# Kernel tuning notes

Measured on AMD Instinct MI355X. Metric: run time of the kernel, lower is better.

Reference implementation:

```python
import jax, jax.numpy as jnp
import numpy as np

D_MODEL = 1024
HEADS = 16
D_HEAD = D_MODEL // HEADS
LN_EPS = 1e-6


def setup_inputs() -> dict:
    key = jax.random.key(0)
    ks = jax.random.split(key, 7)
    B, S = 4, 2048
    scale = 1.0 / np.sqrt(D_MODEL)
    return {
        "q": jax.random.normal(ks[0], (B, S, D_MODEL), jnp.float32),
        "k": jax.random.normal(ks[1], (B, S, D_MODEL), jnp.float32),
        "v": jax.random.normal(ks[2], (B, S, D_MODEL), jnp.float32),
        "Wq": jax.random.normal(ks[3], (D_MODEL, D_MODEL), jnp.float32) * scale,
        "Wk": jax.random.normal(ks[4], (D_MODEL, D_MODEL), jnp.float32) * scale,
        "Wv": jax.random.normal(ks[5], (D_MODEL, D_MODEL), jnp.float32) * scale,
        "Wo": jax.random.normal(ks[6], (D_MODEL, D_MODEL), jnp.float32) * scale,
        "ln_gamma": jnp.ones((D_MODEL,), jnp.float32),
        "ln_beta": jnp.zeros((D_MODEL,), jnp.float32),
    }


def reference(q, k, v, Wq, Wk, Wv, Wo, ln_gamma, ln_beta):
    B, S, _ = q.shape
    residual = q
    # torch Linear (no bias): y = x @ W.T
    qh = (q @ Wq.T).reshape(B, S, HEADS, D_HEAD).transpose(0, 2, 1, 3)
    kh = (k @ Wk.T).reshape(B, S, HEADS, D_HEAD).transpose(0, 2, 1, 3)
    vh = (v @ Wv.T).reshape(B, S, HEADS, D_HEAD).transpose(0, 2, 1, 3)
    # scaled dot-product attention (no mask, dropout=0)
    att = jnp.einsum("bhsd,bhtd->bhst", qh, kh) / jnp.sqrt(jnp.float32(D_HEAD))
    att = jax.nn.softmax(att, axis=-1)
    ctx = jnp.einsum("bhst,bhtd->bhsd", att, vh)  # (B,H,S,Dh)
    ctx = ctx.transpose(0, 2, 1, 3).reshape(B, S, D_MODEL)
    out = ctx @ Wo.T
    out = out + residual
    # LayerNorm, eps=1e-6
    mu = out.mean(axis=-1, keepdims=True)
    var = out.var(axis=-1, keepdims=True)
    out = (out - mu) * jax.lax.rsqrt(var + LN_EPS) * ln_gamma + ln_beta
    return out
```

## Files before the change

kernel.cpp:

```cpp
#include <hip/hip_runtime.h>
#include <hip/hip_bf16.h>

#define DEVI __device__ __forceinline__

typedef unsigned int u32;
typedef unsigned short u16;
typedef __bf16 bf16_t;
typedef bf16_t bf16x8 __attribute__((ext_vector_type(8)));
typedef bf16_t bf16x4 __attribute__((ext_vector_type(4)));
typedef float f32x4 __attribute__((ext_vector_type(4)));
typedef u32 u32x4 __attribute__((ext_vector_type(4)));
typedef u32 u32x2 __attribute__((ext_vector_type(2)));

DEVI u16 f2bf(float f) {
    u32 u = __builtin_bit_cast(u32, f);
    u = (u + 0x7FFFu + ((u >> 16) & 1u)) >> 16;
    return (u16)u;
}

DEVI u32 pack2bf(float lo, float hi) {
    u32 d;
    asm("v_cvt_pk_bf16_f32 %0, %1, %2" : "=v"(d) : "v"(lo), "v"(hi));
    return d;
}

DEVI float fast_exp2(float x) { return __builtin_amdgcn_exp2f(x); }

typedef __attribute__((address_space(3))) u32 as3_u32;
typedef __attribute__((address_space(1))) u32 as1_u32;

DEVI void gld_lds16(const u16* gsrc, u16* ldst) {
    __builtin_amdgcn_global_load_lds((as1_u32*)gsrc, (as3_u32*)ldst, 16, 0, 0);
}

struct CastArgs {
    const float* src[7];
    u16* dst[7];
    int n[7];
};

__global__ __launch_bounds__(256) void cast_kernel(CastArgs a) {
    int z = blockIdx.y;
    int i = (blockIdx.x * 256 + threadIdx.x) * 8;
    if (i >= a.n[z]) return;
    const float* s = a.src[z] + i;
    float4 f0 = ((const float4*)s)[0];
    float4 f1 = ((const float4*)s)[1];
    u32x4 o;
    o.x = pack2bf(f0.x, f0.y);
    o.y = pack2bf(f0.z, f0.w);
    o.z = pack2bf(f1.x, f1.y);
    o.w = pack2bf(f1.z, f1.w);
    *(u32x4*)(a.dst[z] + i) = o;
}

DEVI void gemm_core(const u16* __restrict__ Ag, const u16* __restrict__ Wg,
                    u16* As, u16* Bs, f32x4 acc[4][4],
                    int tid, int mw, int nw, int q, int cl)
{
    const int K = 1024;
    for (int k0 = 0; k0 < K; k0 += 64) {
        if (k0) __syncthreads();
        #pragma unroll
        for (int pass = 0; pass < 4; ++pass) {
            int id = pass * 256 + tid;
            int r = id >> 3, cp = id & 7, cg = cp ^ (r & 7);
            gld_lds16(Ag + (size_t)r * K + k0 + cg * 8, &As[id * 8]);
            gld_lds16(Wg + (size_t)r * K + k0 + cg * 8, &Bs[id * 8]);
        }
        __syncthreads();
        #pragma unroll
        for (int kh = 0; kh < 2; ++kh) {
            bf16x8 af[4], bfr[4];
            #pragma unroll
            for (int i = 0; i < 4; ++i) {
                int R = mw + i * 16 + cl;
                af[i] = *(const bf16x8*)&As[R * 64 + (((kh * 4 + q) ^ (cl & 7)) * 8)];
            }
            #pragma unroll
            for (int j = 0; j < 4; ++j) {
                int R = nw + j * 16 + cl;
                bfr[j] = *(const bf16x8*)&Bs[R * 64 + (((kh * 4 + q) ^ (cl & 7)) * 8)];
            }
            #pragma unroll
            for (int i = 0; i < 4; ++i)
                #pragma unroll
                for (int j = 0; j < 4; ++j)
                    acc[i][j] = __builtin_amdgcn_mfma_f32_16x16x32_bf16(af[i], bfr[j], acc[i][j], 0, 0, 0);
        }
    }
}

struct QKVArgs { const u16* A[3]; const u16* W[3]; u16* out[3]; };

__global__ __launch_bounds__(256) void qkv_gemm(QKVArgs ga) {
    __shared__ __align__(16) u16 As[128 * 64];
    __shared__ __align__(16) u16 Bs[128 * 64];
    int lin = blockIdx.x;
    int xcd = lin & 7, idx = lin >> 3;
    int wid = xcd * 192 + idx;
    int z = wid >> 9;
    int rem = wid & 511;
    int m0 = (rem >> 3) * 128;
    int n0 = (rem & 7) * 128;

    int tid = threadIdx.x;
    int lane = tid & 63, w = tid >> 6;
    int q = lane >> 4, cl = lane & 15;
    int mw = (w >> 1) * 64, nw = (w & 1) * 64;

    f32x4 acc[4][4] = {};
    const u16* Ag = ga.A[z] + (size_t)m0 * 1024;
    const u16* Wg = ga.W[z] + (size_t)n0 * 1024;
    gemm_core(Ag, Wg, As, Bs, acc, tid, mw, nw, q, cl);

    u16* outb = ga.out[z];
    if (z == 0) {
        const float SC = 0.125f * 1.44269504088896340736f;
        #pragma unroll
        for (int i = 0; i < 4; ++i) {
            int row = m0 + mw + i * 16 + q * 4;
            #pragma unroll
            for (int j = 0; j < 4; ++j) {
                int col = n0 + nw + j * 16 + cl;
                #pragma unroll
                for (int r = 0; r < 4; ++r)
                    outb[(size_t)(row + r) * 1024 + col] = f2bf(acc[i][j][r] * SC);
            }
        }
    } else if (z == 1) {
        #pragma unroll
        for (int i = 0; i < 4; ++i) {
            int row = m0 + mw + i * 16 + q * 4;
            #pragma unroll
            for (int j = 0; j < 4; ++j) {
                int col = n0 + nw + j * 16 + cl;
                #pragma unroll
                for (int r = 0; r < 4; ++r)
                    outb[(size_t)(row + r) * 1024 + col] = f2bf(acc[i][j][r]);
            }
        }
    } else {
        #pragma unroll
        for (int i = 0; i < 4; ++i) {
            int mrow = m0 + mw + i * 16 + q * 4;
            int bb = mrow >> 11, s = mrow & 2047;
            #pragma unroll
            for (int j = 0; j < 4; ++j) {
                int n = n0 + nw + j * 16 + cl;
                u32x2 pk;
                pk.x = pack2bf(acc[i][j][0], acc[i][j][1]);
                pk.y = pack2bf(acc[i][j][2], acc[i][j][3]);
                *(u32x2*)&outb[(size_t)(bb * 1024 + n) * 2048 + s] = pk;
            }
        }
    }
}

__global__ __launch_bounds__(256) void gemm_wo(
    const u16* __restrict__ A, const u16* __restrict__ W,
    float* __restrict__ outf, const float* __restrict__ resid)
{
    __shared__ __align__(16) u16 As[128 * 64];
    __shared__ __align__(16) u16 Bs[128 * 64];
    int lin = blockIdx.x;
    int xcd = lin & 7, idx = lin >> 3;
    int wid = xcd * 64 + idx;
    int m0 = (wid >> 3) * 128;
    int n0 = (wid & 7) * 128;

    int tid = threadIdx.x;
    int lane = tid & 63, w = tid >> 6;
    int q = lane >> 4, cl = lane & 15;
    int mw = (w >> 1) * 64, nw = (w & 1) * 64;

    f32x4 acc[4][4] = {};
    const u16* Ag = A + (size_t)m0 * 1024;
    const u16* Wg = W + (size_t)n0 * 1024;
    gemm_core(Ag, Wg, As, Bs, acc, tid, mw, nw, q, cl);

    #pragma unroll
    for (int i = 0; i < 4; ++i) {
        int row = m0 + mw + i * 16 + q * 4;
        #pragma unroll
        for (int j = 0; j < 4; ++j) {
            int col = n0 + nw + j * 16 + cl;
            #pragma unroll
            for (int r = 0; r < 4; ++r) {
                size_t idx2 = (size_t)(row + r) * 1024 + col;
                outf[idx2] = acc[i][j][r] + resid[idx2];
            }
        }
    }
}


DEVI int kperm64(int r) {
    return (r & 32) | ((r & 12) << 1) | ((r & 16) >> 2) | (r & 3);
}

__global__ __launch_bounds__(256, 4) void attn_kernel(
    const u16* __restrict__ Qp, const u16* __restrict__ Kp,
    const u16* __restrict__ Vt, u16* __restrict__ ctx)
{
    __shared__ __align__(16) u16 Ks[2][64 * 64];
    __shared__ __align__(16) u16 Vs[2][64 * 64];

    int tid = threadIdx.x;
    int lane = tid & 63, w = tid >> 6;
    int q = lane >> 4, cl = lane & 15;

    int linear = blockIdx.x + (blockIdx.y << 4);
    int xcd = linear & 7, j = linear >> 3;
    int bh = xcd * 8 + (j >> 4);
    int qt = j & 15;
    int b = bh >> 4, h = bh & 15;

    const u16* Qg = Qp + (size_t)(b * 2048 + qt * 128) * 1024 + h * 64;
    const u16* Kg = Kp + (size_t)(b * 2048) * 1024 + h * 64;
    const u16* Vg = Vt + (size_t)(b * 1024 + h * 64) * 2048;

    bf16x8 aq[2][2];
    #pragma unroll
    for (int tr = 0; tr < 2; ++tr)
        #pragma unroll
        for (int kk = 0; kk < 2; ++kk)
            aq[tr][kk] = *(const bf16x8*)&Qg[(size_t)(w * 32 + tr * 16 + cl) * 1024 + kk * 32 + q * 8];

    u32x4 ou; ou.x = 0x3F803F80u; ou.y = 0x3F803F80u; ou.z = 0x3F803F80u; ou.w = 0x3F803F80u;
    const bf16x8 ones = __builtin_bit_cast(bf16x8, ou);

    f32x4 oacc[2][4] = {};
    f32x4 lacc[2] = {};

    auto stage = [&](int kt, int bufsel) {
        #pragma unroll
        for (int p = 0; p < 2; ++p) {
            int cid = p * 256 + tid;
            int r = cid >> 3, cp = cid & 7, cg = cp ^ (r & 7);
            gld_lds16(Kg + (size_t)(kt * 64 + kperm64(r)) * 1024 + cg * 8, &Ks[bufsel][cid * 8]);
        }
        #pragma unroll
        for (int p = 0; p < 2; ++p) {
            int cid = p * 256 + tid;
            int r = cid >> 3, cp = cid & 7, cg = cp ^ (r & 7);
            gld_lds16(Vg + (size_t)r * 2048 + kt * 64 + cg * 8, &Vs[bufsel][cid * 8]);
        }
    };

    stage(0, 0);
    asm volatile("s_waitcnt vmcnt(0)" ::: "memory");
    __builtin_amdgcn_s_barrier();
    __builtin_amdgcn_sched_barrier(0);

    for (int kt = 0; kt < 32; ++kt) {
        int cur = kt & 1;
        if (kt < 31) stage(kt + 1, cur ^ 1);
        __builtin_amdgcn_sched_barrier(0);

        const u16* KsC = &Ks[cur][0];
        const u16* VsC = &Vs[cur][0];

        bf16x8 pb[2][2];
        #pragma unroll
        for (int t = 0; t < 2; ++t) {
            int krA = t * 32 + cl, krB = t * 32 + 16 + cl;
            bf16x8 ka0 = *(const bf16x8*)&KsC[krA * 64 + ((q ^ (cl & 7)) * 8)];
            bf16x8 ka1 = *(const bf16x8*)&KsC[krA * 64 + (((4 + q) ^ (cl & 7)) * 8)];
            bf16x8 kb0 = *(const bf16x8*)&KsC[krB * 64 + ((q ^ (cl & 7)) * 8)];
            bf16x8 kb1 = *(const bf16x8*)&KsC[krB * 64 + (((4 + q) ^ (cl & 7)) * 8)];
            #pragma unroll
            for (int tr = 0; tr < 2; ++tr) {
                f32x4 sA = {0.f, 0.f, 0.f, 0.f};
                f32x4 sB = {0.f, 0.f, 0.f, 0.f};
                __builtin_amdgcn_s_setprio(1);
                sA = __builtin_amdgcn_mfma_f32_16x16x32_bf16(ka0, aq[tr][0], sA, 0, 0, 0);
                sA = __builtin_amdgcn_mfma_f32_16x16x32_bf16(ka1, aq[tr][1], sA, 0, 0, 0);
                sB = __builtin_amdgcn_mfma_f32_16x16x32_bf16(kb0, aq[tr][0], sB, 0, 0, 0);
                sB = __builtin_amdgcn_mfma_f32_16x16x32_bf16(kb1, aq[tr][1], sB, 0, 0, 0);
                __builtin_amdgcn_s_setprio(0);
                u32x4 pk;
                pk.x = pack2bf(fast_exp2(sA[0]), fast_exp2(sA[1]));
                pk.y = pack2bf(fast_exp2(sA[2]), fast_exp2(sA[3]));
                pk.z = pack2bf(fast_exp2(sB[0]), fast_exp2(sB[1]));
                pk.w = pack2bf(fast_exp2(sB[2]), fast_exp2(sB[3]));
                pb[tr][t] = __builtin_bit_cast(bf16x8, pk);
            }
        }

        #pragma unroll
        for (int t = 0; t < 2; ++t) {
            #pragma unroll
            for (int td = 0; td < 4; ++td) {
                int d = td * 16 + cl;
                bf16x8 bv = *(const bf16x8*)&VsC[d * 64 + (((t * 4 + q) ^ (cl & 7)) * 8)];
                __builtin_amdgcn_s_setprio(1);
                oacc[0][td] = __builtin_amdgcn_mfma_f32_16x16x32_bf16(pb[0][t], bv, oacc[0][td], 0, 0, 0);
                oacc[1][td] = __builtin_amdgcn_mfma_f32_16x16x32_bf16(pb[1][t], bv, oacc[1][td], 0, 0, 0);
                __builtin_amdgcn_s_setprio(0);
            }
            __builtin_amdgcn_s_setprio(1);
            lacc[0] = __builtin_amdgcn_mfma_f32_16x16x32_bf16(pb[0][t], ones, lacc[0], 0, 0, 0);
            lacc[1] = __builtin_amdgcn_mfma_f32_16x16x32_bf16(pb[1][t], ones, lacc[1], 0, 0, 0);
            __builtin_amdgcn_s_setprio(0);
        }

        asm volatile("s_waitcnt vmcnt(0)" ::: "memory");
        __builtin_amdgcn_s_barrier();
        __builtin_amdgcn_sched_barrier(0);
    }

    u16* Cg = ctx + (size_t)(b * 2048 + qt * 128) * 1024 + h * 64;
    #pragma unroll
    for (int tr = 0; tr < 2; ++tr) {
        #pragma unroll
        for (int r = 0; r < 4; ++r) {
            float ir = 1.f / lacc[tr][r];
            int srow = w * 32 + tr * 16 + q * 4 + r;
            #pragma unroll
            for (int td = 0; td < 4; ++td)
                Cg[(size_t)srow * 1024 + td * 16 + cl] = f2bf(oacc[tr][td][r] * ir);
        }
    }
}

__global__ __launch_bounds__(256) void ln_kernel(float* __restrict__ out,
    const float* __restrict__ gamma, const float* __restrict__ beta)
{
    int lane = threadIdx.x & 63;
    int row = blockIdx.x * 4 + (threadIdx.x >> 6);
    float* x = out + (size_t)row * 1024;
    float4 v0 = *(const float4*)&x[lane * 4];
    float4 v1 = *(const float4*)&x[256 + lane * 4];
    float4 v2 = *(const float4*)&x[512 + lane * 4];
    float4 v3 = *(const float4*)&x[768 + lane * 4];
    float s  = (v0.x + v0.y + v0.z + v0.w) + (v1.x + v1.y + v1.z + v1.w)
             + (v2.x + v2.y + v2.z + v2.w) + (v3.x + v3.y + v3.z + v3.w);
    float ss = (v0.x*v0.x + v0.y*v0.y + v0.z*v0.z + v0.w*v0.w)
             + (v1.x*v1.x + v1.y*v1.y + v1.z*v1.z + v1.w*v1.w)
             + (v2.x*v2.x + v2.y*v2.y + v2.z*v2.z + v2.w*v2.w)
             + (v3.x*v3.x + v3.y*v3.y + v3.z*v3.z + v3.w*v3.w);
    #pragma unroll
    for (int off = 1; off < 64; off <<= 1) {
        s += __shfl_xor(s, off, 64);
        ss += __shfl_xor(ss, off, 64);
    }
    float mean = s * (1.f / 1024.f);
    float var = ss * (1.f / 1024.f) - mean * mean;
    float rstd = rsqrtf(var + 1e-6f);
    float4 g0 = *(const float4*)&gamma[lane * 4];
    float4 g1 = *(const float4*)&gamma[256 + lane * 4];
    float4 g2 = *(const float4*)&gamma[512 + lane * 4];
    float4 g3 = *(const float4*)&gamma[768 + lane * 4];
    float4 b0 = *(const float4*)&beta[lane * 4];
    float4 b1 = *(const float4*)&beta[256 + lane * 4];
    float4 b2 = *(const float4*)&beta[512 + lane * 4];
    float4 b3 = *(const float4*)&beta[768 + lane * 4];
    float4 y;
    y.x = (v0.x - mean) * rstd * g0.x + b0.x;
    y.y = (v0.y - mean) * rstd * g0.y + b0.y;
    y.z = (v0.z - mean) * rstd * g0.z + b0.z;
    y.w = (v0.w - mean) * rstd * g0.w + b0.w;
    *(float4*)&x[lane * 4] = y;
    y.x = (v1.x - mean) * rstd * g1.x + b1.x;
    y.y = (v1.y - mean) * rstd * g1.y + b1.y;
    y.z = (v1.z - mean) * rstd * g1.z + b1.z;
    y.w = (v1.w - mean) * rstd * g1.w + b1.w;
    *(float4*)&x[256 + lane * 4] = y;
    y.x = (v2.x - mean) * rstd * g2.x + b2.x;
    y.y = (v2.y - mean) * rstd * g2.y + b2.y;
    y.z = (v2.z - mean) * rstd * g2.z + b2.z;
    y.w = (v2.w - mean) * rstd * g2.w + b2.w;
    *(float4*)&x[512 + lane * 4] = y;
    y.x = (v3.x - mean) * rstd * g3.x + b3.x;
    y.y = (v3.y - mean) * rstd * g3.y + b3.y;
    y.z = (v3.z - mean) * rstd * g3.z + b3.z;
    y.w = (v3.w - mean) * rstd * g3.w + b3.w;
    *(float4*)&x[768 + lane * 4] = y;
}

extern "C" void kernel_launch(void* const* d_in, const int* in_sizes, int n_in,
                              void* d_out, int out_size, void* d_ws, size_t ws_size,
                              hipStream_t stream) {
    const float* q  = (const float*)d_in[0];
    const float* k  = (const float*)d_in[1];
    const float* v  = (const float*)d_in[2];
    const float* Wq = (const float*)d_in[3];
    const float* Wk = (const float*)d_in[4];
    const float* Wv = (const float*)d_in[5];
    const float* Wo = (const float*)d_in[6];
    const float* gamma = (const float*)d_in[7];
    const float* beta  = (const float*)d_in[8];
    float* out = (float*)d_out;

    u16* qb  = (u16*)d_ws;
    u16* kb  = qb + 8388608;
    u16* vb  = kb + 8388608;
    u16* Wqb = vb + 8388608;
    u16* Wkb = Wqb + 1048576;
    u16* Wvb = Wkb + 1048576;
    u16* Wob = Wvb + 1048576;
    u16* Qp  = Wob + 1048576;
    u16* Kp  = Qp + 8388608;
    u16* Vtb = Kp + 8388608;
    u16* ctx = Vtb + 8388608;

    CastArgs ca;
    ca.src[0] = q;  ca.src[1] = k;  ca.src[2] = v;
    ca.src[3] = Wq; ca.src[4] = Wk; ca.src[5] = Wv; ca.src[6] = Wo;
    ca.dst[0] = qb;  ca.dst[1] = kb;  ca.dst[2] = vb;
    ca.dst[3] = Wqb; ca.dst[4] = Wkb; ca.dst[5] = Wvb; ca.dst[6] = Wob;
    ca.n[0] = ca.n[1] = ca.n[2] = 8388608;
    ca.n[3] = ca.n[4] = ca.n[5] = ca.n[6] = 1048576;

    cast_kernel<<<dim3(4096, 7), 256, 0, stream>>>(ca);

    QKVArgs ga;
    ga.A[0] = qb;  ga.A[1] = kb;  ga.A[2] = vb;
    ga.W[0] = Wqb; ga.W[1] = Wkb; ga.W[2] = Wvb;
    ga.out[0] = Qp; ga.out[1] = Kp; ga.out[2] = Vtb;
    qkv_gemm<<<dim3(1536), 256, 0, stream>>>(ga);

    attn_kernel<<<dim3(16, 64), 256, 0, stream>>>(Qp, Kp, Vtb, ctx);

    gemm_wo<<<dim3(512), 256, 0, stream>>>(ctx, Wob, out, q);

    ln_kernel<<<2048, 256, 0, stream>>>(out, gamma, beta);
}
```

Baseline: 327.7 us.

## Software-pipeline attention so QK of the next tile overlaps PV of the current

Restructures the attention main loop so that the QK^T/exp step for key tile kt runs in the same phase as the P·V step for tile kt-1. It is unrolled by two with ping-pong P fragment registers (pbA/pbB), plus a prologue and an epilogue. V shared memory goes from double to triple buffering so the V tile being consumed stays live one phase longer. The aim is to interleave exp/pack VALU work with independent MFMA work and hide latency, at the cost of more registers and 8 KB more LDS per block, which could limit occupancy under the 4-blocks launch bound.

Result: slower. 339.6 us (+3.7%).

```diff
diff --git a/kernel.cpp b/kernel.cpp
--- a/kernel.cpp
+++ b/kernel.cpp
@@ -199,12 +199,63 @@
     return (r & 32) | ((r & 12) << 1) | ((r & 16) >> 2) | (r & 3);
 }
 
+DEVI void qk_tile(const u16* __restrict__ KsC, const bf16x8 (&aq)[2][2],
+                  int q, int cl, bf16x8 (&pb)[2][2])
+{
+    #pragma unroll
+    for (int t = 0; t < 2; ++t) {
+        int krA = t * 32 + cl, krB = t * 32 + 16 + cl;
+        bf16x8 ka0 = *(const bf16x8*)&KsC[krA * 64 + ((q ^ (cl & 7)) * 8)];
+        bf16x8 ka1 = *(const bf16x8*)&KsC[krA * 64 + (((4 + q) ^ (cl & 7)) * 8)];
+        bf16x8 kb0 = *(const bf16x8*)&KsC[krB * 64 + ((q ^ (cl & 7)) * 8)];
+        bf16x8 kb1 = *(const bf16x8*)&KsC[krB * 64 + (((4 + q) ^ (cl & 7)) * 8)];
+        #pragma unroll
+        for (int tr = 0; tr < 2; ++tr) {
+            f32x4 sA = {0.f, 0.f, 0.f, 0.f};
+            f32x4 sB = {0.f, 0.f, 0.f, 0.f};
+            __builtin_amdgcn_s_setprio(1);
+            sA = __builtin_amdgcn_mfma_f32_16x16x32_bf16(ka0, aq[tr][0], sA, 0, 0, 0);
+            sA = __builtin_amdgcn_mfma_f32_16x16x32_bf16(ka1, aq[tr][1], sA, 0, 0, 0);
+            sB = __builtin_amdgcn_mfma_f32_16x16x32_bf16(kb0, aq[tr][0], sB, 0, 0, 0);
+            sB = __builtin_amdgcn_mfma_f32_16x16x32_bf16(kb1, aq[tr][1], sB, 0, 0, 0);
+            __builtin_amdgcn_s_setprio(0);
+            u32x4 pk;
+            pk.x = pack2bf(fast_exp2(sA[0]), fast_exp2(sA[1]));
+            pk.y = pack2bf(fast_exp2(sA[2]), fast_exp2(sA[3]));
+            pk.z = pack2bf(fast_exp2(sB[0]), fast_exp2(sB[1]));
+            pk.w = pack2bf(fast_exp2(sB[2]), fast_exp2(sB[3]));
+            pb[tr][t] = __builtin_bit_cast(bf16x8, pk);
+        }
+    }
+}
+
+DEVI void pv_tile(const u16* __restrict__ VsC, const bf16x8 (&pb)[2][2], bf16x8 ones,
+                  int q, int cl, f32x4 (&oacc)[2][4], f32x4 (&lacc)[2])
+{
+    #pragma unroll
+    for (int t = 0; t < 2; ++t) {
+        #pragma unroll
+        for (int td = 0; td < 4; ++td) {
+            int d = td * 16 + cl;
+            bf16x8 bv = *(const bf16x8*)&VsC[d * 64 + (((t * 4 + q) ^ (cl & 7)) * 8)];
+            __builtin_amdgcn_s_setprio(1);
+            oacc[0][td] = __builtin_amdgcn_mfma_f32_16x16x32_bf16(pb[0][t], bv, oacc[0][td], 0, 0, 0);
+            oacc[1][td] = __builtin_amdgcn_mfma_f32_16x16x32_bf16(pb[1][t], bv, oacc[1][td], 0, 0, 0);
+            __builtin_amdgcn_s_setprio(0);
+        }
+        __builtin_amdgcn_s_setprio(1);
+        lacc[0] = __builtin_amdgcn_mfma_f32_16x16x32_bf16(pb[0][t], ones, lacc[0], 0, 0, 0);
+        lacc[1] = __builtin_amdgcn_mfma_f32_16x16x32_bf16(pb[1][t], ones, lacc[1], 0, 0, 0);
+        __builtin_amdgcn_s_setprio(0);
+    }
+}
+
 __global__ __launch_bounds__(256, 4) void attn_kernel(
     const u16* __restrict__ Qp, const u16* __restrict__ Kp,
     const u16* __restrict__ Vt, u16* __restrict__ ctx)
 {
     __shared__ __align__(16) u16 Ks[2][64 * 64];
-    __shared__ __align__(16) u16 Vs[2][64 * 64];
+    __shared__ __align__(16) u16 Vs[3][64 * 64];
 
     int tid = threadIdx.x;
     int lane = tid & 63, w = tid >> 6;
@@ -232,83 +283,54 @@
 
     f32x4 oacc[2][4] = {};
     f32x4 lacc[2] = {};
-
-    auto stage = [&](int kt, int bufsel) {
+    bf16x8 pbA[2][2], pbB[2][2];
+
+    auto stage = [&](int kt, int kb, int vb) {
         #pragma unroll
         for (int p = 0; p < 2; ++p) {
             int cid = p * 256 + tid;
             int r = cid >> 3, cp = cid & 7, cg = cp ^ (r & 7);
-            gld_lds16(Kg + (size_t)(kt * 64 + kperm64(r)) * 1024 + cg * 8, &Ks[bufsel][cid * 8]);
+            gld_lds16(Kg + (size_t)(kt * 64 + kperm64(r)) * 1024 + cg * 8, &Ks[kb][cid * 8]);
         }
         #pragma unroll
         for (int p = 0; p < 2; ++p) {
             int cid = p * 256 + tid;
             int r = cid >> 3, cp = cid & 7, cg = cp ^ (r & 7);
-            gld_lds16(Vg + (size_t)r * 2048 + kt * 64 + cg * 8, &Vs[bufsel][cid * 8]);
+            gld_lds16(Vg + (size_t)r * 2048 + kt * 64 + cg * 8, &Vs[vb][cid * 8]);
         }
     };
 
-    stage(0, 0);
+    stage(0, 0, 0);
     asm volatile("s_waitcnt vmcnt(0)" ::: "memory");
     __builtin_amdgcn_s_barrier();
     __builtin_amdgcn_sched_barrier(0);
 
-    for (int kt = 0; kt < 32; ++kt) {
-        int cur = kt & 1;
-        if (kt < 31) stage(kt + 1, cur ^ 1);
+    stage(1, 1, 1);
+    __builtin_amdgcn_sched_barrier(0);
+    qk_tile(&Ks[0][0], aq, q, cl, pbA);
+    asm volatile("s_waitcnt vmcnt(0)" ::: "memory");
+    __builtin_amdgcn_s_barrier();
+    __builtin_amdgcn_sched_barrier(0);
+
+    for (int kt = 1; kt < 31; kt += 2) {
+        stage(kt + 1, (kt + 1) & 1, (kt + 1) % 3);
         __builtin_amdgcn_sched_barrier(0);
-
-        const u16* KsC = &Ks[cur][0];
-        const u16* VsC = &Vs[cur][0];
-
-        bf16x8 pb[2][2];
-        #pragma unroll
-        for (int t = 0; t < 2; ++t) {
-            int krA = t * 32 + cl, krB = t * 32 + 16 + cl;
-            bf16x8 ka0 = *(const bf16x8*)&KsC[krA * 64 + ((q ^ (cl & 7)) * 8)];
-            bf16x8 ka1 = *(const bf16x8*)&KsC[krA * 64 + (((4 + q) ^ (cl & 7)) * 8)];
-            bf16x8 kb0 = *(const bf16x8*)&KsC[krB * 64 + ((q ^ (cl & 7)) * 8)];
-            bf16x8 kb1 = *(const bf16x8*)&KsC[krB * 64 + (((4 + q) ^ (cl & 7)) * 8)];
-            #pragma unroll
-            for (int tr = 0; tr < 2; ++tr) {
-                f32x4 sA = {0.f, 0.f, 0.f, 0.f};
-                f32x4 sB = {0.f, 0.f, 0.f, 0.f};
-                __builtin_amdgcn_s_setprio(1);
-                sA = __builtin_amdgcn_mfma_f32_16x16x32_bf16(ka0, aq[tr][0], sA, 0, 0, 0);
-                sA = __builtin_amdgcn_mfma_f32_16x16x32_bf16(ka1, aq[tr][1], sA, 0, 0, 0);
-                sB = __builtin_amdgcn_mfma_f32_16x16x32_bf16(kb0, aq[tr][0], sB, 0, 0, 0);
-                sB = __builtin_amdgcn_mfma_f32_16x16x32_bf16(kb1, aq[tr][1], sB, 0, 0, 0);
-                __builtin_amdgcn_s_setprio(0);
-                u32x4 pk;
-                pk.x = pack2bf(fast_exp2(sA[0]), fast_exp2(sA[1]));
-                pk.y = pack2bf(fast_exp2(sA[2]), fast_exp2(sA[3]));
-                pk.z = pack2bf(fast_exp2(sB[0]), fast_exp2(sB[1]));
-                pk.w = pack2bf(fast_exp2(sB[2]), fast_exp2(sB[3]));
-                pb[tr][t] = __builtin_bit_cast(bf16x8, pk);
-            }
-        }
-
-        #pragma unroll
-        for (int t = 0; t < 2; ++t) {
-            #pragma unroll
-            for (int td = 0; td < 4; ++td) {
-                int d = td * 16 + cl;
-                bf16x8 bv = *(const bf16x8*)&VsC[d * 64 + (((t * 4 + q) ^ (cl & 7)) * 8)];
-                __builtin_amdgcn_s_setprio(1);
-                oacc[0][td] = __builtin_amdgcn_mfma_f32_16x16x32_bf16(pb[0][t], bv, oacc[0][td], 0, 0, 0);
-                oacc[1][td] = __builtin_amdgcn_mfma_f32_16x16x32_bf16(pb[1][t], bv, oacc[1][td], 0, 0, 0);
-                __builtin_amdgcn_s_setprio(0);
-            }
-            __builtin_amdgcn_s_setprio(1);
-            lacc[0] = __builtin_amdgcn_mfma_f32_16x16x32_bf16(pb[0][t], ones, lacc[0], 0, 0, 0);
-            lacc[1] = __builtin_amdgcn_mfma_f32_16x16x32_bf16(pb[1][t], ones, lacc[1], 0, 0, 0);
-            __builtin_amdgcn_s_setprio(0);
-        }
-
+        qk_tile(&Ks[kt & 1][0], aq, q, cl, pbB);
+        pv_tile(&Vs[(kt - 1) % 3][0], pbA, ones, q, cl, oacc, lacc);
         asm volatile("s_waitcnt vmcnt(0)" ::: "memory");
         __builtin_amdgcn_s_barrier();
         __builtin_amdgcn_sched_barrier(0);
-    }
+        stage(kt + 2, (kt + 2) & 1, (kt + 2) % 3);
+        __builtin_amdgcn_sched_barrier(0);
+        qk_tile(&Ks[(kt + 1) & 1][0], aq, q, cl, pbA);
+        pv_tile(&Vs[kt % 3][0], pbB, ones, q, cl, oacc, lacc);
+        asm volatile("s_waitcnt vmcnt(0)" ::: "memory");
+        __builtin_amdgcn_s_barrier();
+        __builtin_amdgcn_sched_barrier(0);
+    }
+    qk_tile(&Ks[1][0], aq, q, cl, pbB);
+    pv_tile(&Vs[0][0], pbA, ones, q, cl, oacc, lacc);
+    pv_tile(&Vs[1][0], pbB, ones, q, cl, oacc, lacc);
 
     u16* Cg = ctx + (size_t)(b * 2048 + qt * 128) * 1024 + h * 64;
     #pragma unroll
```
